# Performance work log

Hardware: AMD Instinct MI355X
Metric: run time of the kernel (lower is better)

Reference implementation:

```python
import jax, jax.numpy as jnp
import numpy as np

U = 64  # LSTM_UNITS

def _lstm(xt, kernel, rec, bias):
    # xt: [B, T, 4U]; keras LSTM gate order i, f, g(c), o
    B = xt.shape[0]
    h0 = jnp.zeros((B, U), xt.dtype)
    c0 = jnp.zeros((B, U), xt.dtype)
    def step(carry, x):
        h, c = carry
        z = x @ kernel + h @ rec + bias  # [B, 4U]
        i, f, g, o = jnp.split(z, 4, axis=-1)
        i = jax.nn.sigmoid(i); f = jax.nn.sigmoid(f)
        g = jnp.tanh(g); o = jax.nn.sigmoid(o)
        c = f * c + i * g
        h = o * jnp.tanh(c)
        return (h, c), h
    _, hs = jax.lax.scan(step, (h0, c0), jnp.swapaxes(xt, 0, 1))
    return jnp.swapaxes(hs, 0, 1)  # [B, T, U]

def setup_inputs() -> dict:
    key = jax.random.key(0)
    ks = jax.random.split(key, 12)
    B, T, P = 8, 100, 1000
    pro_id = jax.random.randint(ks[0], (B, T), 0, P, dtype=jnp.int32)
    label = jax.random.randint(ks[1], (B, T), 0, 2, dtype=jnp.int32)
    X = jax.random.normal(ks[2], (P, 2 * U), jnp.float32)
    cos_X = jax.random.uniform(ks[3], (P, P), jnp.float32)
    trimatrix = jnp.tril(jnp.ones((T, T), jnp.float32))  # causal mask [s, t]
    onehot_table = jax.random.normal(ks[4], (2, 4 * U), jnp.float32)
    s = 0.05
    lstm_kernel = jax.random.normal(ks[5], (4 * U, 4 * U), jnp.float32) * s
    lstm_rec = jax.random.normal(ks[6], (U, 4 * U), jnp.float32) * s
    lstm_bias = jnp.zeros((4 * U,), jnp.float32)
    W1 = jax.random.normal(ks[7], (3 * U, 50), jnp.float32) * s
    b1 = jnp.zeros((50,), jnp.float32)
    W2 = jax.random.normal(ks[8], (50, 1), jnp.float32) * s
    b2 = jnp.zeros((1,), jnp.float32)
    return {"pro_id": pro_id, "label": label, "num_pro": P, "X": X,
            "cos_X": cos_X, "trimatrix": trimatrix, "onehot_table": onehot_table,
            "lstm_kernel": lstm_kernel, "lstm_rec": lstm_rec, "lstm_bias": lstm_bias,
            "W1": W1, "b1": b1, "W2": W2, "b2": b2}

def reference(pro_id, label, num_pro, X, cos_X, trimatrix, onehot_table,
              lstm_kernel, lstm_rec, lstm_bias, W1, b1, W2, b2):
    B, T = pro_id.shape
    # one_hot @ X  ==  gather rows of X
    t_X = jnp.tile(X[pro_id], (1, 1, 2))           # [B, T, 4U]
    label_emb = onehot_table[label]                 # [B, T, 4U]
    xt = t_X * label_emb
    ht = _lstm(xt, lstm_kernel, lstm_rec, lstm_bias)  # [B, T, U]
    a = cos_X[pro_id]                               # [B, T, P] (one_hot @ cos_X)
    # ajhj[b,t,p,u] = sum_s tri[s,t] * a[b,s,p] * ht[b,s,u]  (causal weighted sum)
    ajhj = jnp.einsum('bsp,bsu,st->btpu', a, ht, trimatrix)
    XX = jnp.broadcast_to(X[None, None], (B, T, num_pro, 2 * U))
    hatt = jnp.concatenate([ajhj, XX], axis=-1)     # [B, T, P, 3U]
    r = jax.nn.relu(hatt @ W1 + b1)                 # [B, T, P, 50]
    prediction = r @ W2 + b2                        # [B, T, P, 1]
    return prediction
```

## Files before the change

### kernel.cpp

```cpp
#include <hip/hip_runtime.h>
#include <math.h>

#define BB 8
#define TT 100
#define PP 1000
#define NJ 52
#define GROW 56

typedef _Float16 half2v __attribute__((ext_vector_type(2)));

__device__ __forceinline__ half2v as_h2(float f) {
    union { float x; half2v h; } u; u.x = f; return u.h;
}


__global__ __launch_bounds__(256) void k1_xk(const int* __restrict__ pro_id,
    const int* __restrict__ label, const float* __restrict__ X,
    const float* __restrict__ onehot, const float* __restrict__ kern,
    const float* __restrict__ bias, float* __restrict__ xk)
{
    __shared__ __align__(16) float xt[2][256];
    const int j = threadIdx.x;
    const int r0 = blockIdx.x * 2;
#pragma unroll
    for (int r = 0; r < 2; ++r) {
        int pid = pro_id[r0 + r];
        int lab = label[r0 + r];
        xt[r][j] = X[pid * 128 + (j & 127)] * onehot[lab * 256 + j];
    }
    __syncthreads();
    float acc0 = bias[j], acc1 = acc0;
    float kc[8];
#pragma unroll
    for (int i = 0; i < 8; ++i) kc[i] = kern[i * 256 + j];
    for (int kg = 0; kg < 32; ++kg) {
        float kn[8];
        const int kgn = (kg < 31) ? kg + 1 : 31;
#pragma unroll
        for (int i = 0; i < 8; ++i) kn[i] = kern[(kgn * 8 + i) * 256 + j];
        const int k0 = kg * 8;
        float4 xa0 = *(const float4*)&xt[0][k0];
        float4 xa1 = *(const float4*)&xt[0][k0 + 4];
        float4 xb0 = *(const float4*)&xt[1][k0];
        float4 xb1 = *(const float4*)&xt[1][k0 + 4];
        acc0 += xa0.x * kc[0] + xa0.y * kc[1] + xa0.z * kc[2] + xa0.w * kc[3]
              + xa1.x * kc[4] + xa1.y * kc[5] + xa1.z * kc[6] + xa1.w * kc[7];
        acc1 += xb0.x * kc[0] + xb0.y * kc[1] + xb0.z * kc[2] + xb0.w * kc[3]
              + xb1.x * kc[4] + xb1.y * kc[5] + xb1.z * kc[6] + xb1.w * kc[7];
#pragma unroll
        for (int i = 0; i < 8; ++i) kc[i] = kn[i];
    }
    xk[(r0 + 0) * 256 + j] = acc0;
    xk[(r0 + 1) * 256 + j] = acc1;
}

__global__ __launch_bounds__(256, 1) void mid(const float* __restrict__ xk,
    const float* __restrict__ rec, const float* __restrict__ W1,
    const float* __restrict__ X, const float* __restrict__ b1,
    float* __restrict__ G, float* __restrict__ XcT)
{
    __shared__ __align__(16) float smem[14720];
    const int tid = threadIdx.x;

    if (blockIdx.x < 8) {
        float* h_all  = smem;
        float* hwork  = smem + 6400;
        float* w1s    = smem + 6432;
        const int b = blockIdx.x;

        if (tid >= 64) {
            for (int idx = tid - 64; idx < 3200; idx += 192) {
                int u2 = idx / 50, jj = idx - u2 * 50;
                w1s[u2 * 52 + jj] = W1[idx];
            }
        }

        if (tid < 64) {
            const int u = tid;
            half2v rp[4][32];
#pragma unroll
            for (int m = 0; m < 32; ++m) {
#pragma unroll
                for (int g2 = 0; g2 < 4; ++g2) {
                    float r0 = rec[(2 * m) * 256 + g2 * 64 + u];
                    float r1 = rec[(2 * m + 1) * 256 + g2 * 64 + u];
                    half2v pv; pv.x = (_Float16)r0; pv.y = (_Float16)r1;
                    rp[g2][m] = pv;
                }
            }
            ((_Float16*)hwork)[u] = (_Float16)0.f;

            const float* xkb = xk + b * TT * 256;
            float xi0 = xkb[u],           xf0 = xkb[64 + u],
                  xg0 = xkb[128 + u],     xo0 = xkb[192 + u];
            float xi1 = xkb[256 + u],     xf1 = xkb[256 + 64 + u],
                  xg1 = xkb[256 + 128 + u], xo1 = xkb[256 + 192 + u];
            float xi2 = xkb[512 + u],     xf2 = xkb[512 + 64 + u],
                  xg2 = xkb[512 + 128 + u], xo2 = xkb[512 + 192 + u];
            float c = 0.f;

            for (int t = 0; t < TT; ++t) {
                float zi = xi0, zf = xf0, zg = xg0, zo = xo0;
                xi0 = xi1; xf0 = xf1; xg0 = xg1; xo0 = xo1;
                xi1 = xi2; xf1 = xf2; xg1 = xg2; xo1 = xo2;
                int tn = (t + 3 < TT) ? t + 3 : TT - 1;
                const float* xp = xkb + tn * 256;
                xi2 = xp[u]; xf2 = xp[64 + u]; xg2 = xp[128 + u]; xo2 = xp[192 + u];

                const float4* hw4 = (const float4*)hwork;
#pragma unroll
                for (int ch = 0; ch < 8; ++ch) {
                    float4 hv = hw4[ch];
                    half2v p0 = as_h2(hv.x), p1 = as_h2(hv.y),
                           p2 = as_h2(hv.z), p3 = as_h2(hv.w);
                    zi = __builtin_amdgcn_fdot2(p0, rp[0][ch * 4 + 0], zi, false);
                    zf = __builtin_amdgcn_fdot2(p0, rp[1][ch * 4 + 0], zf, false);
                    zg = __builtin_amdgcn_fdot2(p0, rp[2][ch * 4 + 0], zg, false);
                    zo = __builtin_amdgcn_fdot2(p0, rp[3][ch * 4 + 0], zo, false);
                    zi = __builtin_amdgcn_fdot2(p1, rp[0][ch * 4 + 1], zi, false);
                    zf = __builtin_amdgcn_fdot2(p1, rp[1][ch * 4 + 1], zf, false);
                    zg = __builtin_amdgcn_fdot2(p1, rp[2][ch * 4 + 1], zg, false);
                    zo = __builtin_amdgcn_fdot2(p1, rp[3][ch * 4 + 1], zo, false);
                    zi = __builtin_amdgcn_fdot2(p2, rp[0][ch * 4 + 2], zi, false);
                    zf = __builtin_amdgcn_fdot2(p2, rp[1][ch * 4 + 2], zf, false);
                    zg = __builtin_amdgcn_fdot2(p2, rp[2][ch * 4 + 2], zg, false);
                    zo = __builtin_amdgcn_fdot2(p2, rp[3][ch * 4 + 2], zo, false);
                    zi = __builtin_amdgcn_fdot2(p3, rp[0][ch * 4 + 3], zi, false);
                    zf = __builtin_amdgcn_fdot2(p3, rp[1][ch * 4 + 3], zf, false);
                    zg = __builtin_amdgcn_fdot2(p3, rp[2][ch * 4 + 3], zg, false);
                    zo = __builtin_amdgcn_fdot2(p3, rp[3][ch * 4 + 3], zo, false);
                }
                float gi = 1.f / (1.f + __expf(-zi));
                float gf = 1.f / (1.f + __expf(-zf));
                float gg = 2.f / (1.f + __expf(-2.f * zg)) - 1.f;
                float go = 1.f / (1.f + __expf(-zo));
                c = gf * c + gi * gg;
                float h = go * (2.f / (1.f + __expf(-2.f * c)) - 1.f);
                h_all[t * 64 + u] = h;
                ((_Float16*)hwork)[u] = (_Float16)h;
            }
        }
        __syncthreads();

        const int brow0 = b * TT;
        for (int idx = tid; idx < TT * 13; idx += 256) {
            int row = idx / 13;
            int m = idx - row * 13;
            int j = 4 * m;
            const float* hrow = &h_all[row * 64];
            float ax = 0.f, ay = 0.f, az = 0.f, aw = 0.f;
#pragma unroll
            for (int u4 = 0; u4 < 16; ++u4) {
                float4 hv  = *(const float4*)&hrow[4 * u4];
                float4 w0  = *(const float4*)&w1s[(4 * u4 + 0) * 52 + j];
                float4 w1v = *(const float4*)&w1s[(4 * u4 + 1) * 52 + j];
                float4 w2  = *(const float4*)&w1s[(4 * u4 + 2) * 52 + j];
                float4 w3  = *(const float4*)&w1s[(4 * u4 + 3) * 52 + j];
                ax += hv.x * w0.x + hv.y * w1v.x + hv.z * w2.x + hv.w * w3.x;
                ay += hv.x * w0.y + hv.y * w1v.y + hv.z * w2.y + hv.w * w3.y;
                az += hv.x * w0.z + hv.y * w1v.z + hv.z * w2.z + hv.w * w3.z;
                aw += hv.x * w0.w + hv.y * w1v.w + hv.z * w2.w + hv.w * w3.w;
            }
            if (m == 12) { az = 0.f; aw = 0.f; }
            *(float4*)&G[(brow0 + row) * GROW + j] = make_float4(ax, ay, az, aw);
        }
    } else {
        float* Xs  = smem;
        float* W1T = smem + 8320;
        const int p0 = (blockIdx.x - 8) * 64;
        for (int idx = tid; idx < 6400; idx += 256) {
            int k = idx & 127, jj = idx >> 7;
            W1T[jj * 128 + k] = W1[(64 + k) * 50 + jj];
        }
#pragma unroll
        for (int r = 0; r < 8; ++r) {
            int flat = (tid + 256 * r) * 4;
            int i = flat >> 7;
            int k = flat & 127;
            int p = p0 + i;
            float4 v = make_float4(0.f, 0.f, 0.f, 0.f);
            if (p < PP) v = *(const float4*)&X[p * 128 + k];
            Xs[(k + 0) * 65 + i] = v.x;
            Xs[(k + 1) * 65 + i] = v.y;
            Xs[(k + 2) * 65 + i] = v.z;
            Xs[(k + 3) * 65 + i] = v.w;
        }
        __syncthreads();
        const int ploc = tid & 63;
        const int j0 = tid >> 6;
        float acc[13];
#pragma unroll
        for (int m = 0; m < 13; ++m) {
            int jj = j0 * 13 + m;
            acc[m] = (jj < 50) ? b1[jj] : 0.f;
        }
        for (int k4 = 0; k4 < 32; ++k4) {
            const int k = 4 * k4;
            float x0 = Xs[(k + 0) * 65 + ploc];
            float x1 = Xs[(k + 1) * 65 + ploc];
            float x2 = Xs[(k + 2) * 65 + ploc];
            float x3 = Xs[(k + 3) * 65 + ploc];
#pragma unroll
            for (int m = 0; m < 13; ++m) {
                int jj = j0 * 13 + m;
                if (jj < 50) {
                    float4 wv = *(const float4*)&W1T[jj * 128 + k];
                    acc[m] += x0 * wv.x + x1 * wv.y + x2 * wv.z + x3 * wv.w;
                }
            }
        }
        int p = p0 + ploc;
        if (p < PP) {
#pragma unroll
            for (int m = 0; m < 13; ++m) {
                int jj = j0 * 13 + m;
                if (jj < 50) XcT[jj * PP + p] = acc[m];
            }
        }
        for (int idx = tid; idx < 6 * 64; idx += 256) {
            int r = 50 + (idx >> 6);
            int pp = p0 + (idx & 63);
            if (pp < PP) XcT[r * PP + pp] = 0.f;
        }
    }
}

__global__ __launch_bounds__(256) void k4_main(const int* __restrict__ pro_id,
    const float* __restrict__ cos_X, const float* __restrict__ XcT,
    const float* __restrict__ G, const float* __restrict__ W2,
    const float* __restrict__ b2, float* __restrict__ out)
{
    __shared__ __align__(16) float Gs[TT * GROW];
    __shared__ float w2s[NJ];
    __shared__ int spid[TT];
    const int b = blockIdx.z;
    const int p = blockIdx.y * 256 + threadIdx.x;
    const int ci = blockIdx.x;
    const int t0 = ci * 7;
    const int t1 = (t0 + 7 < TT) ? (t0 + 7) : TT;
    const bool valid = p < PP;
    const int pc = valid ? p : 0;
    const int tid = threadIdx.x;

    {
        const float4* Gg = (const float4*)(G + b * TT * GROW);
        float4* Gd = (float4*)Gs;
        for (int idx = tid; idx < TT * GROW / 4; idx += 256) Gd[idx] = Gg[idx];
        if (tid < TT) spid[tid] = pro_id[b * TT + tid];
        if (tid < NJ) w2s[tid] = (tid < 50) ? W2[tid] : 0.f;
    }

    float V[NJ];
#pragma unroll
    for (int jj = 0; jj < NJ; ++jj) V[jj] = XcT[jj * PP + pc];
    const float b2v = b2[0];
    __syncthreads();

    const float* cb = cos_X + pc;
    float a0 = cb[spid[99] * PP];
    float a1 = cb[spid[98] * PP];
    float a2 = cb[spid[97] * PP];
    float a3 = cb[spid[96] * PP];

    for (int s = TT - 1; s >= t0; --s) {
        float a = a0; a0 = a1; a1 = a2; a2 = a3;
        int sp = s - 4;
        if (sp < t0) sp = t0;
        a3 = cb[spid[sp] * PP];
        const float4* G4 = (const float4*)&Gs[s * GROW];
#pragma unroll
        for (int jv = 0; jv < 13; ++jv) {
            float4 gv = G4[jv];
            V[4 * jv + 0] += a * gv.x;
            V[4 * jv + 1] += a * gv.y;
            V[4 * jv + 2] += a * gv.z;
            V[4 * jv + 3] += a * gv.w;
        }
        if (s < t1) {
            float acc = b2v;
#pragma unroll
            for (int jv = 0; jv < 13; ++jv) {
                float4 wv = *(const float4*)&w2s[4 * jv];
                acc += wv.x * fmaxf(V[4 * jv + 0], 0.f)
                     + wv.y * fmaxf(V[4 * jv + 1], 0.f)
                     + wv.z * fmaxf(V[4 * jv + 2], 0.f)
                     + wv.w * fmaxf(V[4 * jv + 3], 0.f);
            }
            if (valid) out[(b * TT + s) * PP + p] = acc;
        }
    }
}

extern "C" void kernel_launch(void* const* d_in, const int* in_sizes, int n_in,
                              void* d_out, int out_size, void* d_ws, size_t ws_size,
                              hipStream_t stream)
{
    const int* pro_id  = (const int*)d_in[0];
    const int* label   = (const int*)d_in[1];
    const float* X     = (const float*)d_in[3];
    const float* cos_X = (const float*)d_in[4];
    const float* onehot = (const float*)d_in[6];
    const float* lk    = (const float*)d_in[7];
    const float* lr    = (const float*)d_in[8];
    const float* lb    = (const float*)d_in[9];
    const float* W1    = (const float*)d_in[10];
    const float* b1    = (const float*)d_in[11];
    const float* W2    = (const float*)d_in[12];
    const float* b2    = (const float*)d_in[13];

    float* ws  = (float*)d_ws;
    float* xk  = ws;
    float* XcT = ws + 204800;
    float* G   = ws + 260800;
    float* out = (float*)d_out;

    hipLaunchKernelGGL(k1_xk,  dim3(400),      dim3(256), 0, stream,
                       pro_id, label, X, onehot, lk, lb, xk);
    hipLaunchKernelGGL(mid,    dim3(24),       dim3(256), 0, stream,
                       xk, lr, W1, X, b1, G, XcT);
    hipLaunchKernelGGL(k4_main,dim3(15, 4, 8), dim3(256), 0, stream,
                       pro_id, cos_X, XcT, G, W2, b2, out);
}
```

Measured before the change: 198.5 us.

## Remove redundant causal recompute in k4 by giving each block the full time loop

The main kernel no longer splits the time axis into 15 chunks that each recompute the suffix accumulation from s=99 down to their own start. Each block now walks all 100 steps once and writes every output row, removing the redundant accumulate work. G rows are streamed from global memory into registers with one-step prefetch instead of being staged in shared memory, and W2 is held in registers. The grid shrinks from 480 to 32 blocks, so far fewer CUs are occupied and each block carries a long serial chain of dependent gathers and stores.

```diff
diff --git a/kernel.cpp b/kernel.cpp
--- a/kernel.cpp
+++ b/kernel.cpp
@@ -91,11 +91,11 @@
             ((_Float16*)hwork)[u] = (_Float16)0.f;
 
             const float* xkb = xk + b * TT * 256;
-            float xi0 = xkb[u],           xf0 = xkb[64 + u],
-                  xg0 = xkb[128 + u],     xo0 = xkb[192 + u];
-            float xi1 = xkb[256 + u],     xf1 = xkb[256 + 64 + u],
+            float xi0 = xkb[u],             xf0 = xkb[64 + u],
+                  xg0 = xkb[128 + u],       xo0 = xkb[192 + u];
+            float xi1 = xkb[256 + u],       xf1 = xkb[256 + 64 + u],
                   xg1 = xkb[256 + 128 + u], xo1 = xkb[256 + 192 + u];
-            float xi2 = xkb[512 + u],     xf2 = xkb[512 + 64 + u],
+            float xi2 = xkb[512 + u],       xf2 = xkb[512 + 64 + u],
                   xg2 = xkb[512 + 128 + u], xo2 = xkb[512 + 192 + u];
             float c = 0.f;
 
@@ -230,30 +230,24 @@
     const float* __restrict__ G, const float* __restrict__ W2,
     const float* __restrict__ b2, float* __restrict__ out)
 {
-    __shared__ __align__(16) float Gs[TT * GROW];
-    __shared__ float w2s[NJ];
     __shared__ int spid[TT];
-    const int b = blockIdx.z;
-    const int p = blockIdx.y * 256 + threadIdx.x;
-    const int ci = blockIdx.x;
-    const int t0 = ci * 7;
-    const int t1 = (t0 + 7 < TT) ? (t0 + 7) : TT;
+    const int b = blockIdx.y;
+    const int p = blockIdx.x * 256 + threadIdx.x;
     const bool valid = p < PP;
     const int pc = valid ? p : 0;
     const int tid = threadIdx.x;
 
-    {
-        const float4* Gg = (const float4*)(G + b * TT * GROW);
-        float4* Gd = (float4*)Gs;
-        for (int idx = tid; idx < TT * GROW / 4; idx += 256) Gd[idx] = Gg[idx];
-        if (tid < TT) spid[tid] = pro_id[b * TT + tid];
-        if (tid < NJ) w2s[tid] = (tid < 50) ? W2[tid] : 0.f;
-    }
+    if (tid < TT) spid[tid] = pro_id[b * TT + tid];
+
+    float4 w2r[13];
+#pragma unroll
+    for (int jv = 0; jv < 12; ++jv) w2r[jv] = *(const float4*)&W2[4 * jv];
+    w2r[12] = make_float4(W2[48], W2[49], 0.f, 0.f);
+    const float b2v = b2[0];
 
     float V[NJ];
 #pragma unroll
     for (int jj = 0; jj < NJ; ++jj) V[jj] = XcT[jj * PP + pc];
-    const float b2v = b2[0];
     __syncthreads();
 
     const float* cb = cos_X + pc;
@@ -262,32 +256,40 @@
     float a2 = cb[spid[97] * PP];
     float a3 = cb[spid[96] * PP];
 
-    for (int s = TT - 1; s >= t0; --s) {
+    const float4* Gb = (const float4*)(G + b * TT * GROW);
+    float4 Gn[13];
+#pragma unroll
+    for (int jv = 0; jv < 13; ++jv) Gn[jv] = Gb[99 * 14 + jv];
+
+    float* outb = out + b * TT * PP + p;
+
+    for (int s = TT - 1; s >= 0; --s) {
+        float4 Gc[13];
+#pragma unroll
+        for (int jv = 0; jv < 13; ++jv) Gc[jv] = Gn[jv];
+        int sn = (s > 0) ? s - 1 : 0;
+#pragma unroll
+        for (int jv = 0; jv < 13; ++jv) Gn[jv] = Gb[sn * 14 + jv];
+
         float a = a0; a0 = a1; a1 = a2; a2 = a3;
-        int sp = s - 4;
-        if (sp < t0) sp = t0;
+        int sp = (s >= 4) ? s - 4 : 0;
         a3 = cb[spid[sp] * PP];
-        const float4* G4 = (const float4*)&Gs[s * GROW];
+
+        float acc = b2v;
 #pragma unroll
         for (int jv = 0; jv < 13; ++jv) {
-            float4 gv = G4[jv];
+            float4 gv = Gc[jv];
             V[4 * jv + 0] += a * gv.x;
             V[4 * jv + 1] += a * gv.y;
             V[4 * jv + 2] += a * gv.z;
             V[4 * jv + 3] += a * gv.w;
-        }
-        if (s < t1) {
-            float acc = b2v;
-#pragma unroll
-            for (int jv = 0; jv < 13; ++jv) {
-                float4 wv = *(const float4*)&w2s[4 * jv];
-                acc += wv.x * fmaxf(V[4 * jv + 0], 0.f)
-                     + wv.y * fmaxf(V[4 * jv + 1], 0.f)
-                     + wv.z * fmaxf(V[4 * jv + 2], 0.f)
-                     + wv.w * fmaxf(V[4 * jv + 3], 0.f);
-            }
-            if (valid) out[(b * TT + s) * PP + p] = acc;
-        }
+            float4 wv = w2r[jv];
+            acc += wv.x * fmaxf(V[4 * jv + 0], 0.f)
+                 + wv.y * fmaxf(V[4 * jv + 1], 0.f)
+                 + wv.z * fmaxf(V[4 * jv + 2], 0.f)
+                 + wv.w * fmaxf(V[4 * jv + 3], 0.f);
+        }
+        if (valid) outb[s * PP] = acc;
     }
 }
 
@@ -314,10 +316,10 @@
     float* G   = ws + 260800;
     float* out = (float*)d_out;
 
-    hipLaunchKernelGGL(k1_xk,  dim3(400),      dim3(256), 0, stream,
+    hipLaunchKernelGGL(k1_xk,  dim3(400),    dim3(256), 0, stream,
                        pro_id, label, X, onehot, lk, lb, xk);
-    hipLaunchKernelGGL(mid,    dim3(24),       dim3(256), 0, stream,
+    hipLaunchKernelGGL(mid,    dim3(24),     dim3(256), 0, stream,
                        xk, lr, W1, X, b1, G, XcT);
-    hipLaunchKernelGGL(k4_main,dim3(15, 4, 8), dim3(256), 0, stream,
+    hipLaunchKernelGGL(k4_main,dim3(4, 8),   dim3(256), 0, stream,
                        pro_id, cos_X, XcT, G, W2, b2, out);
 }
```

Result: slower. 205.6 us (+3.6%).
